# Kernel optimization log

Measured on AMD Instinct MI355X. Metric: run time of the kernel, lower is better.

## Reference

```python
import jax, jax.numpy as jnp
import numpy as np

B, TXT_T, MEL_T, N_MEL = 8, 200, 800, 80
PAD_MAG = 1.0e12


def setup_inputs() -> dict:
    key = jax.random.key(0)
    k1, k2, k3, k4 = jax.random.split(key, 4)
    mu_logvar = jax.random.normal(k1, (B, TXT_T, 2 * N_MEL), dtype=jnp.float32)
    melspec = jax.random.normal(k2, (B, N_MEL, MEL_T), dtype=jnp.float32)
    # lengths are 1-based (indexed as length-1), keep them in [T//2, T]
    text_lengths = jax.random.randint(k3, (B,), TXT_T // 2, TXT_T + 1)
    mel_lengths = jax.random.randint(k4, (B,), MEL_T // 2, MEL_T + 1)
    return {
        "mu_logvar": mu_logvar,
        "melspec": melspec,
        "text_lengths": text_lengths,
        "mel_lengths": mel_lengths,
    }


def _log_prob_matrix(mu_logvar, melspec):
    # melspec: [B, n_mel, mel_T] -> x: [B, 1, mel_T, n_mel]
    x = jnp.transpose(melspec, (0, 2, 1))[:, None, :, :]
    mu = mu_logvar[:, :, :N_MEL][:, :, None, :]       # [B, txt_T, 1, n_mel]
    logvar = mu_logvar[:, :, N_MEL:][:, :, None, :]   # [B, txt_T, 1, n_mel]
    # -0.5 * mean_over_mel( (x-mu)^2 / exp(logvar) + logvar )
    sq = (x - mu) ** 2
    return (-0.5 * (sq * jnp.exp(-logvar) + logvar)).mean(axis=3)  # [B, txt_T, mel_T]


def reference(mu_logvar, melspec, text_lengths, mel_lengths):
    lp = _log_prob_matrix(mu_logvar, melspec)  # [B, txt_T, mel_T]

    # log_alpha column carry, with a leading pad row (index 0 stays -PAD_MAG)
    init = jnp.full((B, TXT_T + 1), -PAD_MAG, dtype=lp.dtype)
    init = init.at[:, 1].set(lp[:, 0, 0])

    def step(a, lp_t):  # a: [B, txt_T+1], lp_t: [B, txt_T]
        # logsumexp over {stay, advance}; original adds 1e-7 to prev values
        new_rows = jnp.logaddexp(a[:, 1:] + 1e-7, a[:, :-1] + 1e-7) + lp_t
        a = a.at[:, 1:].set(new_rows)
        return a, new_rows

    lp_rest = jnp.moveaxis(lp[:, :, 1:], 2, 0)  # [mel_T-1, B, txt_T]
    _, cols = jax.lax.scan(step, init, lp_rest)  # cols: [mel_T-1, B, txt_T]

    log_alpha = jnp.concatenate(
        [init[:, 1:, None], jnp.moveaxis(cols, 0, 2)], axis=2
    )  # [B, txt_T, mel_T]

    b = jnp.arange(B)
    alpha_last = log_alpha[b, text_lengths - 1, mel_lengths - 1]
    alpha_last = alpha_last / mel_lengths.astype(alpha_last.dtype)
    mdn_loss = -alpha_last.mean()
    return mdn_loss, lp
```

## Files before the change

kernel.cpp:

```cpp
#include <hip/hip_runtime.h>
#include <math.h>

#define BB 8
#define TXT_T 200
#define MEL_T 800
#define N_MEL 80
#define LPT_STRIDE 200
#define CH 32
#define LOG2E 1.44269504088896340736f
#define LN2   0.69314718055994530942f
#define EPS2  (1e-7f * LOG2E)
#define NPAD  -1.0e12f

__device__ __forceinline__ float exp2_hw(float x) {
#if __has_builtin(__builtin_amdgcn_exp2f)
    return __builtin_amdgcn_exp2f(x);
#else
    return __expf(LN2 * x);
#endif
}

__device__ __forceinline__ float lse2(float A, float B) {
    float m = fmaxf(A, B);
    float e = exp2_hw(-fabsf(A - B));
    return m + __log2f(1.0f + e);
}

__device__ __forceinline__ float lse3(float A, float B, float C) {
    float m = fmaxf(fmaxf(A, B), C);
    float e = exp2_hw(A - m) + exp2_hw(B - m) + exp2_hw(C - m);
    return m + __log2f(e);
}

__global__ void __launch_bounds__(256) lp_kernel(
        const float* __restrict__ mu_logvar,
        const float* __restrict__ melspec,
        float* __restrict__ out_lp,
        float* __restrict__ lpT) {
    const int bt = blockIdx.x;
    const int b  = bt / TXT_T;
    const int t  = bt % TXT_T;
    const int tid = threadIdx.x;

    __shared__ float s_mu[N_MEL];
    __shared__ float s_ev[N_MEL];
    __shared__ float s_lv[N_MEL];
    __shared__ float s_sumlv;

    if (tid < N_MEL) {
        float mu = mu_logvar[(size_t)bt * (2 * N_MEL) + tid];
        float lv = mu_logvar[(size_t)bt * (2 * N_MEL) + N_MEL + tid];
        s_mu[tid] = mu;
        s_ev[tid] = __expf(-lv);
        s_lv[tid] = lv;
    }
    __syncthreads();
    if (tid == 0) {
        float s = 0.f;
        #pragma unroll
        for (int n = 0; n < N_MEL; ++n) s += s_lv[n];
        s_sumlv = s;
    }
    __syncthreads();

    if (tid < MEL_T / 4) {
        const float4* ms4 = (const float4*)(melspec + (size_t)b * N_MEL * MEL_T);
        float ax = 0.f, ay = 0.f, az = 0.f, aw = 0.f;
        #pragma unroll 8
        for (int n = 0; n < N_MEL; ++n) {
            float4 x = ms4[(size_t)n * (MEL_T / 4) + tid];
            float mu = s_mu[n];
            float ev = s_ev[n];
            float d0 = x.x - mu; ax += d0 * d0 * ev;
            float d1 = x.y - mu; ay += d1 * d1 * ev;
            float d2 = x.z - mu; az += d2 * d2 * ev;
            float d3 = x.w - mu; aw += d3 * d3 * ev;
        }
        const float c = -0.5f / (float)N_MEL;
        float slv = s_sumlv;
        float l0 = c * (ax + slv);
        float l1 = c * (ay + slv);
        float l2 = c * (az + slv);
        float l3 = c * (aw + slv);

        size_t ob = (size_t)bt * MEL_T + tid * 4;
        out_lp[ob + 0] = l0;
        out_lp[ob + 1] = l1;
        out_lp[ob + 2] = l2;
        out_lp[ob + 3] = l3;

        int m0 = tid * 4;
        size_t tb = ((size_t)b * MEL_T + m0) * LPT_STRIDE + t;
        lpT[tb + 0 * LPT_STRIDE] = l0 * LOG2E + EPS2;
        lpT[tb + 1 * LPT_STRIDE] = l1 * LOG2E + EPS2;
        lpT[tb + 2 * LPT_STRIDE] = l2 * LOG2E + EPS2;
        lpT[tb + 3 * LPT_STRIDE] = l3 * LOG2E + EPS2;
    }
}

__device__ __forceinline__ void stage_chunk(const float* g, float* s, int lane) {
    #pragma unroll
    for (int i = 0; i < 25; ++i) {
        __builtin_amdgcn_global_load_lds(
            (const __attribute__((address_space(1))) void*)(g + i * 256 + lane * 4),
            (__attribute__((address_space(3))) void*)(s + i * 256),
            16, 0, 0);
    }
}

#define STEP2L(SB, TLOC, TT) do {                                             \
    float4 p_ = *(const float4*)((SB) + (TLOC) * LPT_STRIDE + j0);            \
    float4 q_ = *(const float4*)((SB) + ((TLOC) + 1) * LPT_STRIDE + j0);      \
    float l1_ = __shfl_up(r3, 1);                                             \
    float l2_ = __shfl_up(r2, 1);                                             \
    float pw_ = __shfl_up(p_.w, 1);                                           \
    if (lane == 0) { l1_ = NPAD; l2_ = NPAD; pw_ = NPAD; }                    \
    if ((TT) == myMel) {          \
        float ga_ = r0, gb_ = l1_, gp_ = p_.x;                                \
        if (acomp == 1) { ga_ = r1; gb_ = r0; gp_ = p_.y; }                   \
        if (acomp == 2) { ga_ = r2; gb_ = r1; gp_ = p_.z; }                   \
        if (acomp == 3) { ga_ = r3; gb_ = r2; gp_ = p_.w; }                   \
        alpha_out[b] = (lse2(ga_, gb_) + gp_) * scale;                        \
    }                                                                         \
    float s0_ = lse2(p_.x, pw_);                                              \
    float s1_ = lse2(p_.y, p_.x);                                             \
    float s2_ = lse2(p_.z, p_.y);                                             \
    float s3_ = lse2(p_.w, p_.z);                                             \
    float x0_ = r0 + p_.x, x1_ = r1 + p_.y, x2_ = r2 + p_.z, x3_ = r3 + p_.w; \
    float y0_ = l1_ + s0_, y1_ = r0 + s1_, y2_ = r1 + s2_, y3_ = r2 + s3_;    \
    float z0_ = l2_ + pw_, z1_ = l1_ + p_.x, z2_ = r0 + p_.y, z3_ = r1 + p_.z;\
    r0 = lse3(x0_, y0_, z0_) + q_.x;                                          \
    r1 = lse3(x1_, y1_, z1_) + q_.y;                                          \
    r2 = lse3(x2_, y2_, z2_) + q_.z;                                          \
    r3 = lse3(x3_, y3_, z3_) + q_.w;                                          \
    if ((TT) + 1 == myMel) {          \
        float v_ = r0;                                                        \
        if (acomp == 1) v_ = r1;                                              \
        if (acomp == 2) v_ = r2;                                              \
        if (acomp == 3) v_ = r3;                                              \
        alpha_out[b] = v_ * scale;                                            \
    }                                                                         \
} while (0)

__global__ void __launch_bounds__(64) scan_kernel(
        const float* __restrict__ lpT,
        const int* __restrict__ text_lengths,
        const int* __restrict__ mel_lengths,
        float* __restrict__ alpha_out) {
    __shared__ float sbuf[2][CH][LPT_STRIDE];
    const int b = blockIdx.x;
    const int lane = threadIdx.x;
    int j0 = lane * 4;
    j0 = j0 > (TXT_T - 4) ? (TXT_T - 4) : j0;

    const int melL1 = mel_lengths[b] - 1;
    const int txtL1 = text_lengths[b] - 1;
    const float scale = LN2 / (float)(melL1 + 1);
    const int acomp = txtL1 & 3;
    const int myMel = (lane == (txtL1 >> 2)) ? melL1 : -1;

    const float* gbase = lpT + (size_t)b * MEL_T * LPT_STRIDE;
    const int clast = melL1 >> 5;

    stage_chunk(gbase,                    &sbuf[0][0][0], lane);
    stage_chunk(gbase + CH * LPT_STRIDE,  &sbuf[1][0][0], lane);

    float r0 = NPAD, r1 = NPAD, r2 = NPAD, r3 = NPAD;

    for (int c = 0; c <= clast; ++c) {
        if (c < clast) { asm volatile("s_waitcnt vmcnt(25)" ::: "memory"); }
        else           { asm volatile("s_waitcnt vmcnt(0)"  ::: "memory"); }

        const float* sb = &sbuf[c & 1][0][0];
        if (c == 0) {
            float4 row0 = *(const float4*)(sb + j0);
            float4 row1 = *(const float4*)(sb + LPT_STRIDE + j0);
            r0 = (lane == 0) ? (row0.x - EPS2) : NPAD;
            float lft = __shfl_up(r3, 1);
            if (lane == 0) lft = NPAD;
            float m0 = lse2(r0, lft) + row1.x;
            float m1 = lse2(r1, r0)  + row1.y;
            float m2 = lse2(r2, r1)  + row1.z;
            float m3 = lse2(r3, r2)  + row1.w;
            r0 = m0; r1 = m1; r2 = m2; r3 = m3;
            #pragma unroll
            for (int m = 0; m < 15; ++m) {
                STEP2L(sb, 2 * m + 2, 2 * m + 2);
            }
        } else {
            const int tbase = 32 * c;
            #pragma unroll
            for (int m = 0; m < 16; ++m) {
                STEP2L(sb, 2 * m, tbase + 2 * m);
            }
        }

        if (c + 2 <= clast) {
            stage_chunk(gbase + (size_t)(c + 2) * CH * LPT_STRIDE,
                        &sbuf[c & 1][0][0], lane);
        }
    }
}

__global__ void finish_kernel(const float* __restrict__ alpha,
                              float* __restrict__ out) {
    float s = 0.f;
    #pragma unroll
    for (int b = 0; b < BB; ++b) s += alpha[b];
    out[0] = -(s / (float)BB);
}

extern "C" void kernel_launch(void* const* d_in, const int* in_sizes, int n_in,
                              void* d_out, int out_size, void* d_ws, size_t ws_size,
                              hipStream_t stream) {
    const float* mu_logvar    = (const float*)d_in[0];
    const float* melspec      = (const float*)d_in[1];
    const int*   text_lengths = (const int*)d_in[2];
    const int*   mel_lengths  = (const int*)d_in[3];
    float* out = (float*)d_out;

    float* alpha = (float*)d_ws;
    float* lpT   = (float*)d_ws + 16;

    lp_kernel<<<BB * TXT_T, 256, 0, stream>>>(mu_logvar, melspec, out + 1, lpT);
    scan_kernel<<<BB, 64, 0, stream>>>(lpT, text_lengths, mel_lengths, alpha);
    finish_kernel<<<1, 1, 0, stream>>>(alpha, out);
}
```

Baseline: 156.1 us.

## Spread scan across 256 threads with one text row each via LDS exchange

The alignment scan moves from one 64-lane wavefront holding four text rows per lane to a 256-thread block holding one row per thread. Neighbour values are now passed through a double-buffered LDS array with a workgroup barrier on every two-step pair, replacing cross-lane shuffles. The lp transpose buffer gets a 256-float row stride and the staging chunk shrinks to 16 rows, loaded cooperatively by the four waves. The aim is to cut the serial per-lane work on the critical path, at the cost of a block-wide barrier and LDS round trip on each dependent step.

```diff
diff --git a/kernel.cpp b/kernel.cpp
--- a/kernel.cpp
+++ b/kernel.cpp
@@ -5,12 +5,15 @@
 #define TXT_T 200
 #define MEL_T 800
 #define N_MEL 80
-#define LPT_STRIDE 200
-#define CH 32
+#define GSTR 256
+#define CH 16
 #define LOG2E 1.44269504088896340736f
 #define LN2   0.69314718055994530942f
 #define EPS2  (1e-7f * LOG2E)
 #define NPAD  -1.0e12f
+
+#define SBAR()       asm volatile("s_barrier" ::: "memory")
+#define WAIT_LGKM0() asm volatile("s_waitcnt lgkmcnt(0)" ::: "memory")
 
 __device__ __forceinline__ float exp2_hw(float x) {
 #if __has_builtin(__builtin_amdgcn_exp2f)
@@ -90,114 +93,115 @@
         out_lp[ob + 3] = l3;
 
         int m0 = tid * 4;
-        size_t tb = ((size_t)b * MEL_T + m0) * LPT_STRIDE + t;
-        lpT[tb + 0 * LPT_STRIDE] = l0 * LOG2E + EPS2;
-        lpT[tb + 1 * LPT_STRIDE] = l1 * LOG2E + EPS2;
-        lpT[tb + 2 * LPT_STRIDE] = l2 * LOG2E + EPS2;
-        lpT[tb + 3 * LPT_STRIDE] = l3 * LOG2E + EPS2;
-    }
-}
-
-__device__ __forceinline__ void stage_chunk(const float* g, float* s, int lane) {
+        size_t tb = ((size_t)(b * MEL_T + m0)) * GSTR + t;
+        lpT[tb + 0 * GSTR] = l0 * LOG2E + EPS2;
+        lpT[tb + 1 * GSTR] = l1 * LOG2E + EPS2;
+        lpT[tb + 2 * GSTR] = l2 * LOG2E + EPS2;
+        lpT[tb + 3 * GSTR] = l3 * LOG2E + EPS2;
+    }
+}
+
+__device__ __forceinline__ void stage16(const float* g, float* s, int w, int lane) {
     #pragma unroll
-    for (int i = 0; i < 25; ++i) {
+    for (int k = 0; k < 4; ++k) {
+        int row = w * 4 + k;
         __builtin_amdgcn_global_load_lds(
-            (const __attribute__((address_space(1))) void*)(g + i * 256 + lane * 4),
-            (__attribute__((address_space(3))) void*)(s + i * 256),
+            (const __attribute__((address_space(1))) void*)(g + row * GSTR + lane * 4),
+            (__attribute__((address_space(3))) void*)(s + row * GSTR),
             16, 0, 0);
     }
 }
 
-#define STEP2L(SB, TLOC, TT) do {                                             \
-    float4 p_ = *(const float4*)((SB) + (TLOC) * LPT_STRIDE + j0);            \
-    float4 q_ = *(const float4*)((SB) + ((TLOC) + 1) * LPT_STRIDE + j0);      \
-    float l1_ = __shfl_up(r3, 1);                                             \
-    float l2_ = __shfl_up(r2, 1);                                             \
-    float pw_ = __shfl_up(p_.w, 1);                                           \
-    if (lane == 0) { l1_ = NPAD; l2_ = NPAD; pw_ = NPAD; }                    \
+#define PAIRL(SB, TLOC, TT) do {                                              \
+    float* rb_ = &rbuf[par][0];                                               \
+    float p_  = (SB)[(TLOC) * GSTR + j];                                      \
+    float pm_ = (SB)[(TLOC) * GSTR + jm1];                                    \
+    float q_  = (SB)[((TLOC) + 1) * GSTR + j];                                \
+    rb_[tid] = r;                                                             \
+    WAIT_LGKM0(); SBAR();                                                     \
+    float rm1_ = rb_[tm1];                                                    \
+    float rm2_ = rb_[tm2];                                                    \
+    if (tid == 0) { rm1_ = NPAD; pm_ = NPAD; }                                \
+    if (tid <= 1) { rm2_ = NPAD; }                                            \
     if ((TT) == myMel) {          \
-        float ga_ = r0, gb_ = l1_, gp_ = p_.x;                                \
-        if (acomp == 1) { ga_ = r1; gb_ = r0; gp_ = p_.y; }                   \
-        if (acomp == 2) { ga_ = r2; gb_ = r1; gp_ = p_.z; }                   \
-        if (acomp == 3) { ga_ = r3; gb_ = r2; gp_ = p_.w; }                   \
-        alpha_out[b] = (lse2(ga_, gb_) + gp_) * scale;                        \
+        alpha_out[b] = (lse2(r, rm1_) + p_) * scale;                          \
     }                                                                         \
-    float s0_ = lse2(p_.x, pw_);                                              \
-    float s1_ = lse2(p_.y, p_.x);                                             \
-    float s2_ = lse2(p_.z, p_.y);                                             \
-    float s3_ = lse2(p_.w, p_.z);                                             \
-    float x0_ = r0 + p_.x, x1_ = r1 + p_.y, x2_ = r2 + p_.z, x3_ = r3 + p_.w; \
-    float y0_ = l1_ + s0_, y1_ = r0 + s1_, y2_ = r1 + s2_, y3_ = r2 + s3_;    \
-    float z0_ = l2_ + pw_, z1_ = l1_ + p_.x, z2_ = r0 + p_.y, z3_ = r1 + p_.z;\
-    r0 = lse3(x0_, y0_, z0_) + q_.x;                                          \
-    r1 = lse3(x1_, y1_, z1_) + q_.y;                                          \
-    r2 = lse3(x2_, y2_, z2_) + q_.z;                                          \
-    r3 = lse3(x3_, y3_, z3_) + q_.w;                                          \
+    float s_ = lse2(p_, pm_);                                                 \
+    float x_ = r + p_;                                                        \
+    float y_ = rm1_ + s_;                                                     \
+    float z_ = rm2_ + pm_;                                                    \
+    r = lse3(x_, y_, z_) + q_;                                                \
     if ((TT) + 1 == myMel) {          \
-        float v_ = r0;                                                        \
-        if (acomp == 1) v_ = r1;                                              \
-        if (acomp == 2) v_ = r2;                                              \
-        if (acomp == 3) v_ = r3;                                              \
-        alpha_out[b] = v_ * scale;                                            \
+        alpha_out[b] = r * scale;                                             \
     }                                                                         \
+    par ^= 1;                                                                 \
 } while (0)
 
-__global__ void __launch_bounds__(64) scan_kernel(
+__global__ void __launch_bounds__(256) scan_kernel(
         const float* __restrict__ lpT,
         const int* __restrict__ text_lengths,
         const int* __restrict__ mel_lengths,
         float* __restrict__ alpha_out) {
-    __shared__ float sbuf[2][CH][LPT_STRIDE];
+    __shared__ float sbuf[2][CH][GSTR];
+    __shared__ float rbuf[2][256];
     const int b = blockIdx.x;
-    const int lane = threadIdx.x;
-    int j0 = lane * 4;
-    j0 = j0 > (TXT_T - 4) ? (TXT_T - 4) : j0;
+    const int tid = threadIdx.x;
+    const int w = tid >> 6;
+    const int lane = tid & 63;
+    const int j   = tid < TXT_T ? tid : (TXT_T - 1);
+    const int jm1 = j > 0 ? j - 1 : 0;
+    const int tm1 = tid > 0 ? tid - 1 : 0;
+    const int tm2 = tid > 1 ? tid - 2 : 0;
 
     const int melL1 = mel_lengths[b] - 1;
     const int txtL1 = text_lengths[b] - 1;
     const float scale = LN2 / (float)(melL1 + 1);
-    const int acomp = txtL1 & 3;
-    const int myMel = (lane == (txtL1 >> 2)) ? melL1 : -1;
-
-    const float* gbase = lpT + (size_t)b * MEL_T * LPT_STRIDE;
-    const int clast = melL1 >> 5;
-
-    stage_chunk(gbase,                    &sbuf[0][0][0], lane);
-    stage_chunk(gbase + CH * LPT_STRIDE,  &sbuf[1][0][0], lane);
-
-    float r0 = NPAD, r1 = NPAD, r2 = NPAD, r3 = NPAD;
+    const int myMel = (tid == txtL1) ? melL1 : -1;
+
+    const float* gbase = lpT + (size_t)b * MEL_T * GSTR;
+    const int clast = melL1 >> 4;
+
+    stage16(gbase,             &sbuf[0][0][0], w, lane);
+    stage16(gbase + CH * GSTR, &sbuf[1][0][0], w, lane);
+
+    float r = NPAD;
+    int par = 0;
 
     for (int c = 0; c <= clast; ++c) {
-        if (c < clast) { asm volatile("s_waitcnt vmcnt(25)" ::: "memory"); }
-        else           { asm volatile("s_waitcnt vmcnt(0)"  ::: "memory"); }
+        if (c < clast) { asm volatile("s_waitcnt vmcnt(4)" ::: "memory"); }
+        else           { asm volatile("s_waitcnt vmcnt(0)" ::: "memory"); }
+        SBAR();
 
         const float* sb = &sbuf[c & 1][0][0];
         if (c == 0) {
-            float4 row0 = *(const float4*)(sb + j0);
-            float4 row1 = *(const float4*)(sb + LPT_STRIDE + j0);
-            r0 = (lane == 0) ? (row0.x - EPS2) : NPAD;
-            float lft = __shfl_up(r3, 1);
-            if (lane == 0) lft = NPAD;
-            float m0 = lse2(r0, lft) + row1.x;
-            float m1 = lse2(r1, r0)  + row1.y;
-            float m2 = lse2(r2, r1)  + row1.z;
-            float m3 = lse2(r3, r2)  + row1.w;
-            r0 = m0; r1 = m1; r2 = m2; r3 = m3;
+            float lp00 = sb[0];
+            r = (tid == 0) ? (lp00 - EPS2) : NPAD;
+            {
+                float* rb_ = &rbuf[par][0];
+                float p_ = sb[GSTR + j];
+                rb_[tid] = r;
+                WAIT_LGKM0(); SBAR();
+                float rm1_ = rb_[tm1];
+                if (tid == 0) rm1_ = NPAD;
+                r = lse2(r, rm1_) + p_;
+                par ^= 1;
+            }
             #pragma unroll
-            for (int m = 0; m < 15; ++m) {
-                STEP2L(sb, 2 * m + 2, 2 * m + 2);
+            for (int m = 1; m < 8; ++m) {
+                PAIRL(sb, 2 * m, 2 * m);
             }
         } else {
-            const int tbase = 32 * c;
+            const int tbase = CH * c;
             #pragma unroll
-            for (int m = 0; m < 16; ++m) {
-                STEP2L(sb, 2 * m, tbase + 2 * m);
+            for (int m = 0; m < 8; ++m) {
+                PAIRL(sb, 2 * m, tbase + 2 * m);
             }
         }
 
+        WAIT_LGKM0(); SBAR();
         if (c + 2 <= clast) {
-            stage_chunk(gbase + (size_t)(c + 2) * CH * LPT_STRIDE,
-                        &sbuf[c & 1][0][0], lane);
+            stage16(gbase + (size_t)(c + 2) * CH * GSTR,
+                    &sbuf[c & 1][0][0], w, lane);
         }
     }
 }
@@ -220,9 +224,9 @@
     float* out = (float*)d_out;
 
     float* alpha = (float*)d_ws;
-    float* lpT   = (float*)d_ws + 16;
+    float* lpT   = (float*)d_ws + 64;
 
     lp_kernel<<<BB * TXT_T, 256, 0, stream>>>(mu_logvar, melspec, out + 1, lpT);
-    scan_kernel<<<BB, 64, 0, stream>>>(lpT, text_lengths, mel_lengths, alpha);
+    scan_kernel<<<BB, 256, 0, stream>>>(lpT, text_lengths, mel_lengths, alpha);
     finish_kernel<<<1, 1, 0, stream>>>(alpha, out);
 }
```

New measurement: 126.5 us. 19.0% less time.
